# Kernel optimization log

Measured on AMD Instinct MI355X. Metric: run time of the kernel, lower is better.

## Reference

```python
import jax, jax.numpy as jnp
import numpy as np

N_NODES = 100000


def setup_inputs() -> dict:
    key = jax.random.key(0)
    k1, k2, k3, k4, k5 = jax.random.split(key, 5)
    h = jax.random.normal(k1, (N_NODES, 128), dtype=jnp.float32)
    norm = jax.random.uniform(k2, (N_NODES, 1), dtype=jnp.float32)  # D^{-1/2}-style per-node norm
    W = jax.random.normal(k3, (128, 64), dtype=jnp.float32) * 0.05
    b = jnp.zeros((64,), dtype=jnp.float32)
    src = jax.random.randint(k4, (1600000,), 0, N_NODES, dtype=jnp.int32)
    dst = jax.random.randint(k5, (1600000,), 0, N_NODES, dtype=jnp.int32)
    return {"h": h, "norm": norm, "W": W, "b": b, "src": src, "dst": dst}


def reference(h, norm, W, b, src, dst):
    # Dense feature transform: g.ndata['h'] = h @ W   (dropout is identity at inference)
    hw = jnp.matmul(h, W)  # [N, out]
    # Message: src feature scaled by src norm
    msg = hw[src] * norm[src]  # [E, out]
    # Reduce: sum messages into dst, scale by dst norm
    agg = jax.ops.segment_sum(msg, dst, num_segments=N_NODES) * norm  # [N, out]
    out = agg + b
    return jax.nn.relu(out)
```

## Files before the change

### kernel.cpp

```cpp
#include <hip/hip_runtime.h>


typedef unsigned int u32;
typedef unsigned short u16;
typedef __attribute__((ext_vector_type(8))) short s16x8;
typedef __attribute__((ext_vector_type(4))) float f32x4;

#define NB_LOG 6
#define NPB 64
#define CAP 2048
#define MAXB 2048
#define EPB 8192
#define RT 256

__device__ __forceinline__ float bf2f(u16 v) {
  return __uint_as_float(((u32)v) << 16);
}
__device__ __forceinline__ u16 f2bf(float f) {
  u32 u = __float_as_uint(f);
  return (u16)((u + 0x7fffu + ((u >> 16) & 1u)) >> 16);
}
__device__ __forceinline__ void acc_bf16x4(float4& a, uint2 v) {
  a.x += __uint_as_float(v.x << 16);
  a.y += __uint_as_float(v.x & 0xFFFF0000u);
  a.z += __uint_as_float(v.y << 16);
  a.w += __uint_as_float(v.y & 0xFFFF0000u);
}

__global__ __launch_bounds__(256) void wconv(
    const float* __restrict__ W, u16* __restrict__ Wtg, u32* __restrict__ gcur) {
  int o = blockIdx.x * 256 + threadIdx.x;
  int j = o & 7, col = (o >> 3) & 15, kq = (o >> 7) & 3, ks = (o >> 9) & 3,
      ct = (o >> 11) & 3;
  int k = ks * 32 + kq * 8 + j;
  int n = ct * 16 + col;
  Wtg[o] = f2bf(W[k * 64 + n]);
  if (o < MAXB) gcur[o] = 0;
}

__global__ __launch_bounds__(256) void gemm_and_bin(
    const float* __restrict__ h, const float* __restrict__ norm,
    const u16* __restrict__ Wtg, u16* __restrict__ scaledh, int N, int nrb,
    const int* __restrict__ src, const int* __restrict__ dst,
    u32* __restrict__ gcur, u32* __restrict__ bins, int E) {
  __shared__ u32 hist[MAXB];
  __shared__ u32 lbase[MAXB];

  if ((int)blockIdx.x < nrb) {
    int lane = threadIdx.x & 63, wid = threadIdx.x >> 6;
    int col = lane & 15, kq = lane >> 4;

    s16x8 bfrag[4][4];
#pragma unroll
    for (int ct = 0; ct < 4; ++ct)
#pragma unroll
      for (int ks = 0; ks < 4; ++ks) {
        int f = ct * 16 + ks * 4 + kq;
        bfrag[ct][ks] =
            *reinterpret_cast<const s16x8*>(Wtg + ((size_t)(f * 16 + col) * 8));
      }

    int row0 = blockIdx.x * 64 + wid * 16;
    int myrow = row0 + col;
    int ldrow = myrow < N ? myrow : (N - 1);
    const float* __restrict__ hrow = h + (size_t)ldrow * 128 + kq * 8;

    f32x4 acc[4];
#pragma unroll
    for (int ct = 0; ct < 4; ++ct) acc[ct] = (f32x4){0.f, 0.f, 0.f, 0.f};

#pragma unroll
    for (int ks = 0; ks < 4; ++ks) {
      float4 x0 = *reinterpret_cast<const float4*>(hrow + ks * 32);
      float4 x1 = *reinterpret_cast<const float4*>(hrow + ks * 32 + 4);
      s16x8 a;
      a[0] = (short)f2bf(x0.x); a[1] = (short)f2bf(x0.y);
      a[2] = (short)f2bf(x0.z); a[3] = (short)f2bf(x0.w);
      a[4] = (short)f2bf(x1.x); a[5] = (short)f2bf(x1.y);
      a[6] = (short)f2bf(x1.z); a[7] = (short)f2bf(x1.w);
#pragma unroll
      for (int ct = 0; ct < 4; ++ct)
        acc[ct] =
            __builtin_amdgcn_mfma_f32_16x16x32_bf16(a, bfrag[ct][ks], acc[ct], 0, 0, 0);
    }

#pragma unroll
    for (int reg = 0; reg < 4; ++reg) {
      int node = row0 + kq * 4 + reg;
      if (node < N) {
        float nm = norm[node];
#pragma unroll
        for (int ct = 0; ct < 4; ++ct)
          scaledh[(size_t)node * 64 + ct * 16 + col] = f2bf(acc[ct][reg] * nm);
      }
    }
    return;
  }

  int bid = (int)blockIdx.x - nrb;
  int t = threadIdx.x;
  for (int i = t; i < MAXB; i += 256) hist[i] = 0;
  __syncthreads();
  int e0 = bid * EPB;
#pragma unroll 4
  for (int k = 0; k < EPB / 256; ++k) {
    int e = e0 + k * 256 + t;
    if (e < E) atomicAdd(&hist[dst[e] >> NB_LOG], 1u);
  }
  __syncthreads();
  for (int i = t; i < MAXB; i += 256) {
    u32 c = hist[i];
    lbase[i] = c ? atomicAdd(&gcur[i], c) : 0u;
  }
  __syncthreads();
  for (int i = t; i < MAXB; i += 256) hist[i] = 0;
  __syncthreads();
#pragma unroll 4
  for (int k = 0; k < EPB / 256; ++k) {
    int e = e0 + k * 256 + t;
    if (e < E) {
      int d = dst[e], s = src[e];
      int bk = d >> NB_LOG;
      u32 p = lbase[bk] + atomicAdd(&hist[bk], 1u);
      if (p < CAP)
        bins[(size_t)bk * CAP + p] = ((u32)s << NB_LOG) | (u32)(d & (NPB - 1));
    }
  }
}

__global__ __launch_bounds__(RT) void bucket_reduce(
    const u16* __restrict__ scaledh, const u32* __restrict__ bins,
    const u32* __restrict__ gcur, const float* __restrict__ norm,
    const float4* __restrict__ bias4, float* __restrict__ out, int N) {
  __shared__ u32 hist[NPB];
  __shared__ u32 startp[NPB + 1];
  __shared__ u32 sorted[CAP];
  int bkt = blockIdx.x;
  int t = threadIdx.x, lane = t & 63, wid = t >> 6;
  int cnt = (int)gcur[bkt];
  if (cnt > CAP) cnt = CAP;
  if (t < NPB) hist[t] = 0;
  __syncthreads();

  const u32* __restrict__ my = bins + (size_t)bkt * CAP;
  u32 w[CAP / RT];
  u32 rk[CAP / RT];
#pragma unroll
  for (int k = 0; k < CAP / RT; ++k) {
    int e = k * RT + t;
    w[k] = (e < cnt) ? my[e] : 0xFFFFFFFFu;
  }
#pragma unroll
  for (int k = 0; k < CAP / RT; ++k) {
    if (w[k] != 0xFFFFFFFFu)
      rk[k] = atomicAdd(&hist[w[k] & (NPB - 1)], 1u);
  }
  __syncthreads();
  if (t < NPB) {
    u32 v = hist[t];
    u32 inc = v;
#pragma unroll
    for (int m = 1; m < NPB; m <<= 1) {
      u32 x = __shfl_up(inc, m);
      if (t >= m) inc += x;
    }
    startp[t] = inc - v;
    if (t == NPB - 1) startp[NPB] = inc;
  }
  __syncthreads();
#pragma unroll
  for (int k = 0; k < CAP / RT; ++k) {
    if (w[k] != 0xFFFFFFFFu)
      sorted[startp[w[k] & (NPB - 1)] + rk[k]] = w[k] >> NB_LOG;
  }
  __syncthreads();

  int grp = lane >> 4, c4 = lane & 15;
  float4 bl = bias4[c4];
  int base = bkt << NB_LOG;
  int cm1 = cnt - 1;
#pragma unroll
  for (int round = 0; round < 2; ++round) {
    int rA = (wid << 4) + (round << 3) + grp;
    int rB = rA + 4;
    int jA = (int)startp[rA], eA = (int)startp[rA + 1];
    int jB = (int)startp[rB], eB = (int)startp[rB + 1];
    float4 aA = make_float4(0.f, 0.f, 0.f, 0.f);
    float4 aB = make_float4(0.f, 0.f, 0.f, 0.f);
    while (jA < eA || jB < eB) {
      int iA0 = (int)sorted[min(jA, cm1)];
      int iA1 = (int)sorted[min(jA + 1, cm1)];
      int iB0 = (int)sorted[min(jB, cm1)];
      int iB1 = (int)sorted[min(jB + 1, cm1)];
      uint2 vA0 = *reinterpret_cast<const uint2*>(scaledh + ((size_t)iA0 << 6) + (c4 << 2));
      uint2 vA1 = *reinterpret_cast<const uint2*>(scaledh + ((size_t)iA1 << 6) + (c4 << 2));
      uint2 vB0 = *reinterpret_cast<const uint2*>(scaledh + ((size_t)iB0 << 6) + (c4 << 2));
      uint2 vB1 = *reinterpret_cast<const uint2*>(scaledh + ((size_t)iB1 << 6) + (c4 << 2));
      uint2 z = make_uint2(0u, 0u);
      vA0 = (jA < eA) ? vA0 : z;
      vA1 = (jA + 1 < eA) ? vA1 : z;
      vB0 = (jB < eB) ? vB0 : z;
      vB1 = (jB + 1 < eB) ? vB1 : z;
      acc_bf16x4(aA, vA0);
      acc_bf16x4(aA, vA1);
      acc_bf16x4(aB, vB0);
      acc_bf16x4(aB, vB1);
      jA += 2;
      jB += 2;
    }
    int nodeA = base + rA, nodeB = base + rB;
    if (nodeA < N) {
      float nm = norm[nodeA];
      float4 o;
      o.x = fmaxf(fmaf(aA.x, nm, bl.x), 0.f);
      o.y = fmaxf(fmaf(aA.y, nm, bl.y), 0.f);
      o.z = fmaxf(fmaf(aA.z, nm, bl.z), 0.f);
      o.w = fmaxf(fmaf(aA.w, nm, bl.w), 0.f);
      *reinterpret_cast<float4*>(out + (size_t)nodeA * 64 + (c4 << 2)) = o;
    }
    if (nodeB < N) {
      float nm = norm[nodeB];
      float4 o;
      o.x = fmaxf(fmaf(aB.x, nm, bl.x), 0.f);
      o.y = fmaxf(fmaf(aB.y, nm, bl.y), 0.f);
      o.z = fmaxf(fmaf(aB.z, nm, bl.z), 0.f);
      o.w = fmaxf(fmaf(aB.w, nm, bl.w), 0.f);
      *reinterpret_cast<float4*>(out + (size_t)nodeB * 64 + (c4 << 2)) = o;
    }
  }
}

__global__ __launch_bounds__(256) void zero_out(float4* __restrict__ o4, size_t n4) {
  size_t tid = blockIdx.x * 256 + threadIdx.x;
  size_t stride = (size_t)gridDim.x * 256;
  for (size_t i = tid; i < n4; i += stride) o4[i] = make_float4(0.f, 0.f, 0.f, 0.f);
}

__global__ __launch_bounds__(256) void scatter_edges(
    const u16* __restrict__ scaledh, const int* __restrict__ src,
    const int* __restrict__ dst, float* __restrict__ agg, int E) {
  int lane = threadIdx.x & 63;
  int gwid = (blockIdx.x * 256 + threadIdx.x) >> 6;
  int nw = (gridDim.x * 256) >> 6;
  for (int e = gwid; e < E; e += nw) {
    int s = __builtin_amdgcn_readfirstlane(src[e]);
    int d = __builtin_amdgcn_readfirstlane(dst[e]);
    float v = bf2f(scaledh[(size_t)s * 64 + lane]);
    unsafeAtomicAdd(&agg[(size_t)d * 64 + lane], v);
  }
}

__global__ __launch_bounds__(256) void finalize(
    float4* __restrict__ out4, const float* __restrict__ norm,
    const float4* __restrict__ b4, int N) {
  size_t total4 = (size_t)N * 16;
  size_t tid = blockIdx.x * 256 + threadIdx.x;
  size_t stride = (size_t)gridDim.x * 256;
  for (size_t t = tid; t < total4; t += stride) {
    int i = (int)(t >> 4), q = (int)(t & 15);
    float4 v = out4[t];
    float nm = norm[i];
    float4 bb = b4[q];
    v.x = fmaxf(fmaf(v.x, nm, bb.x), 0.f);
    v.y = fmaxf(fmaf(v.y, nm, bb.y), 0.f);
    v.z = fmaxf(fmaf(v.z, nm, bb.z), 0.f);
    v.w = fmaxf(fmaf(v.w, nm, bb.w), 0.f);
    out4[t] = v;
  }
}

extern "C" void kernel_launch(void* const* d_in, const int* in_sizes, int n_in,
                              void* d_out, int out_size, void* d_ws, size_t ws_size,
                              hipStream_t stream) {
  const float* h    = (const float*)d_in[0];
  const float* norm = (const float*)d_in[1];
  const float* W    = (const float*)d_in[2];
  const float* b    = (const float*)d_in[3];
  const int*   src  = (const int*)d_in[4];
  const int*   dst  = (const int*)d_in[5];

  int N = in_sizes[1];
  int E = in_sizes[4];
  int nbuckets = (N + NPB - 1) >> NB_LOG;
  int nrb = (N + 63) >> 6;
  int nbinb = (E + EPB - 1) / EPB;

  char* ws = (char*)d_ws;
  size_t off = 0;
  u16* scaledh = (u16*)(ws + off); off += (((size_t)N * 64 * 2) + 255) & ~(size_t)255;
  u32* gcur    = (u32*)(ws + off); off += (MAXB * 4 + 255) & ~(size_t)255;
  u16* Wtg     = (u16*)(ws + off); off += (8192 * 2 + 255) & ~(size_t)255;
  u32* bins    = (u32*)(ws + off); off += (size_t)MAXB * CAP * 4;
  size_t needed = off;
  size_t needed_fb = (size_t)((char*)bins - ws);

  if (ws_size >= needed && nbuckets <= MAXB) {
    wconv<<<32, 256, 0, stream>>>(W, Wtg, gcur);
    gemm_and_bin<<<nrb + nbinb, 256, 0, stream>>>(h, norm, Wtg, scaledh, N, nrb,
                                                  src, dst, gcur, bins, E);
    bucket_reduce<<<nbuckets, RT, 0, stream>>>(scaledh, bins, gcur, norm,
                                               (const float4*)b, (float*)d_out, N);
  } else if (ws_size >= needed_fb) {
    float* agg = (float*)d_out;
    wconv<<<32, 256, 0, stream>>>(W, Wtg, gcur);
    gemm_and_bin<<<nrb, 256, 0, stream>>>(h, norm, Wtg, scaledh, N, nrb,
                                          src, dst, gcur, bins, E);
    zero_out<<<1024, 256, 0, stream>>>((float4*)agg, (size_t)N * 16);
    scatter_edges<<<2048, 256, 0, stream>>>(scaledh, src, dst, agg, E);
    finalize<<<1024, 256, 0, stream>>>((float4*)agg, norm, (const float4*)b, N);
  }
}
```

Before: 93.29 us.

## Schedule binning blocks first, shrink edge chunks, keep edges in registers

```diff
diff --git a/kernel.cpp b/kernel.cpp
--- a/kernel.cpp
+++ b/kernel.cpp
@@ -10,7 +10,7 @@
 #define NPB 64
 #define CAP 2048
 #define MAXB 2048
-#define EPB 8192
+#define EPB 2048
 #define RT 256
 
 __device__ __forceinline__ float bf2f(u16 v) {
@@ -40,90 +40,93 @@
 
 __global__ __launch_bounds__(256) void gemm_and_bin(
     const float* __restrict__ h, const float* __restrict__ norm,
-    const u16* __restrict__ Wtg, u16* __restrict__ scaledh, int N, int nrb,
+    const u16* __restrict__ Wtg, u16* __restrict__ scaledh, int N, int nbinb,
     const int* __restrict__ src, const int* __restrict__ dst,
     u32* __restrict__ gcur, u32* __restrict__ bins, int E) {
-  __shared__ u32 hist[MAXB];
+  __shared__ u32 lhist[MAXB];
   __shared__ u32 lbase[MAXB];
 
-  if ((int)blockIdx.x < nrb) {
-    int lane = threadIdx.x & 63, wid = threadIdx.x >> 6;
-    int col = lane & 15, kq = lane >> 4;
-
-    s16x8 bfrag[4][4];
+  if ((int)blockIdx.x < nbinb) {
+    int t = threadIdx.x;
+    for (int i = t; i < MAXB; i += 256) lhist[i] = 0;
+    __syncthreads();
+    int e0 = blockIdx.x * EPB;
+    int s[8], d[8];
+    u32 r[8];
+#pragma unroll
+    for (int k = 0; k < 8; ++k) {
+      int e = e0 + k * 256 + t;
+      bool ok = e < E;
+      s[k] = ok ? src[e] : 0;
+      d[k] = ok ? dst[e] : -1;
+    }
+#pragma unroll
+    for (int k = 0; k < 8; ++k) {
+      if (d[k] >= 0) r[k] = atomicAdd(&lhist[d[k] >> NB_LOG], 1u);
+    }
+    __syncthreads();
+    for (int i = t; i < MAXB; i += 256) {
+      u32 c = lhist[i];
+      lbase[i] = c ? atomicAdd(&gcur[i], c) : 0u;
+    }
+    __syncthreads();
+#pragma unroll
+    for (int k = 0; k < 8; ++k) {
+      if (d[k] >= 0) {
+        int bk = d[k] >> NB_LOG;
+        u32 p = lbase[bk] + r[k];
+        if (p < CAP)
+          bins[(size_t)bk * CAP + p] = ((u32)s[k] << NB_LOG) | (u32)(d[k] & (NPB - 1));
+      }
+    }
+    return;
+  }
+
+  int lane = threadIdx.x & 63, wid = threadIdx.x >> 6;
+  int col = lane & 15, kq = lane >> 4;
+
+  s16x8 bfrag[4][4];
+#pragma unroll
+  for (int ct = 0; ct < 4; ++ct)
+#pragma unroll
+    for (int ks = 0; ks < 4; ++ks) {
+      int f = ct * 16 + ks * 4 + kq;
+      bfrag[ct][ks] =
+          *reinterpret_cast<const s16x8*>(Wtg + ((size_t)(f * 16 + col) * 8));
+    }
+
+  int row0 = ((int)blockIdx.x - nbinb) * 64 + wid * 16;
+  int myrow = row0 + col;
+  int ldrow = myrow < N ? myrow : (N - 1);
+  const float* __restrict__ hrow = h + (size_t)ldrow * 128 + kq * 8;
+
+  f32x4 acc[4];
+#pragma unroll
+  for (int ct = 0; ct < 4; ++ct) acc[ct] = (f32x4){0.f, 0.f, 0.f, 0.f};
+
+#pragma unroll
+  for (int ks = 0; ks < 4; ++ks) {
+    float4 x0 = *reinterpret_cast<const float4*>(hrow + ks * 32);
+    float4 x1 = *reinterpret_cast<const float4*>(hrow + ks * 32 + 4);
+    s16x8 a;
+    a[0] = (short)f2bf(x0.x); a[1] = (short)f2bf(x0.y);
+    a[2] = (short)f2bf(x0.z); a[3] = (short)f2bf(x0.w);
+    a[4] = (short)f2bf(x1.x); a[5] = (short)f2bf(x1.y);
+    a[6] = (short)f2bf(x1.z); a[7] = (short)f2bf(x1.w);
 #pragma unroll
     for (int ct = 0; ct < 4; ++ct)
-#pragma unroll
-      for (int ks = 0; ks < 4; ++ks) {
-        int f = ct * 16 + ks * 4 + kq;
-        bfrag[ct][ks] =
-            *reinterpret_cast<const s16x8*>(Wtg + ((size_t)(f * 16 + col) * 8));
-      }
-
-    int row0 = blockIdx.x * 64 + wid * 16;
-    int myrow = row0 + col;
-    int ldrow = myrow < N ? myrow : (N - 1);
-    const float* __restrict__ hrow = h + (size_t)ldrow * 128 + kq * 8;
-
-    f32x4 acc[4];
-#pragma unroll
-    for (int ct = 0; ct < 4; ++ct) acc[ct] = (f32x4){0.f, 0.f, 0.f, 0.f};
-
-#pragma unroll
-    for (int ks = 0; ks < 4; ++ks) {
-      float4 x0 = *reinterpret_cast<const float4*>(hrow + ks * 32);
-      float4 x1 = *reinterpret_cast<const float4*>(hrow + ks * 32 + 4);
-      s16x8 a;
-      a[0] = (short)f2bf(x0.x); a[1] = (short)f2bf(x0.y);
-      a[2] = (short)f2bf(x0.z); a[3] = (short)f2bf(x0.w);
-      a[4] = (short)f2bf(x1.x); a[5] = (short)f2bf(x1.y);
-      a[6] = (short)f2bf(x1.z); a[7] = (short)f2bf(x1.w);
+      acc[ct] =
+          __builtin_amdgcn_mfma_f32_16x16x32_bf16(a, bfrag[ct][ks], acc[ct], 0, 0, 0);
+  }
+
+#pragma unroll
+  for (int reg = 0; reg < 4; ++reg) {
+    int node = row0 + kq * 4 + reg;
+    if (node < N) {
+      float nm = norm[node];
 #pragma unroll
       for (int ct = 0; ct < 4; ++ct)
-        acc[ct] =
-            __builtin_amdgcn_mfma_f32_16x16x32_bf16(a, bfrag[ct][ks], acc[ct], 0, 0, 0);
-    }
-
-#pragma unroll
-    for (int reg = 0; reg < 4; ++reg) {
-      int node = row0 + kq * 4 + reg;
-      if (node < N) {
-        float nm = norm[node];
-#pragma unroll
-        for (int ct = 0; ct < 4; ++ct)
-          scaledh[(size_t)node * 64 + ct * 16 + col] = f2bf(acc[ct][reg] * nm);
-      }
-    }
-    return;
-  }
-
-  int bid = (int)blockIdx.x - nrb;
-  int t = threadIdx.x;
-  for (int i = t; i < MAXB; i += 256) hist[i] = 0;
-  __syncthreads();
-  int e0 = bid * EPB;
-#pragma unroll 4
-  for (int k = 0; k < EPB / 256; ++k) {
-    int e = e0 + k * 256 + t;
-    if (e < E) atomicAdd(&hist[dst[e] >> NB_LOG], 1u);
-  }
-  __syncthreads();
-  for (int i = t; i < MAXB; i += 256) {
-    u32 c = hist[i];
-    lbase[i] = c ? atomicAdd(&gcur[i], c) : 0u;
-  }
-  __syncthreads();
-  for (int i = t; i < MAXB; i += 256) hist[i] = 0;
-  __syncthreads();
-#pragma unroll 4
-  for (int k = 0; k < EPB / 256; ++k) {
-    int e = e0 + k * 256 + t;
-    if (e < E) {
-      int d = dst[e], s = src[e];
-      int bk = d >> NB_LOG;
-      u32 p = lbase[bk] + atomicAdd(&hist[bk], 1u);
-      if (p < CAP)
-        bins[(size_t)bk * CAP + p] = ((u32)s << NB_LOG) | (u32)(d & (NPB - 1));
+        scaledh[(size_t)node * 64 + ct * 16 + col] = f2bf(acc[ct][reg] * nm);
     }
   }
 }
@@ -296,14 +299,14 @@
 
   if (ws_size >= needed && nbuckets <= MAXB) {
     wconv<<<32, 256, 0, stream>>>(W, Wtg, gcur);
-    gemm_and_bin<<<nrb + nbinb, 256, 0, stream>>>(h, norm, Wtg, scaledh, N, nrb,
+    gemm_and_bin<<<nbinb + nrb, 256, 0, stream>>>(h, norm, Wtg, scaledh, N, nbinb,
                                                   src, dst, gcur, bins, E);
     bucket_reduce<<<nbuckets, RT, 0, stream>>>(scaledh, bins, gcur, norm,
                                                (const float4*)b, (float*)d_out, N);
   } else if (ws_size >= needed_fb) {
     float* agg = (float*)d_out;
     wconv<<<32, 256, 0, stream>>>(W, Wtg, gcur);
-    gemm_and_bin<<<nrb, 256, 0, stream>>>(h, norm, Wtg, scaledh, N, nrb,
+    gemm_and_bin<<<nrb, 256, 0, stream>>>(h, norm, Wtg, scaledh, N, 0,
                                           src, dst, gcur, bins, E);
     zero_out<<<1024, 256, 0, stream>>>((float4*)agg, (size_t)N * 16);
     scatter_edges<<<2048, 256, 0, stream>>>(scaledh, src, dst, agg, E);
```

Result: slower. 101.3 us (+8.5%).
